# Performance work log

Hardware: AMD Instinct MI355X
Metric: run time of the kernel (lower is better)

The kernel has to match this reference:

```python
import jax, jax.numpy as jnp
import numpy as np

N_NODES = 100000
N_EDGES = 1600000
N_GRAPHS = 64
BN_EPS = 1e-5


def setup_inputs() -> dict:
    key = jax.random.key(0)
    ks = jax.random.split(key, 16)
    inp = {
        'x': jax.random.normal(ks[0], (N_NODES, 768), dtype=jnp.float32),
        'edge_index': jax.random.randint(ks[1], (2, N_EDGES), 0, N_NODES, dtype=jnp.int32),
        'batch': jnp.sort(jax.random.randint(ks[2], (N_NODES,), 0, N_GRAPHS, dtype=jnp.int32)),
        'W_in': jax.random.normal(ks[3], (768, 256), dtype=jnp.float32) * 0.02,
        'b_in': jax.random.normal(ks[4], (256,), dtype=jnp.float32) * 0.02,
        'W_g': jax.random.normal(ks[5], (3, 256, 256), dtype=jnp.float32) * 0.05,
        'b_g': jax.random.normal(ks[6], (3, 256), dtype=jnp.float32) * 0.02,
        'bn_gamma': jax.random.uniform(ks[7], (3, 256), dtype=jnp.float32) + 0.5,
        'bn_beta': jax.random.normal(ks[8], (3, 256), dtype=jnp.float32) * 0.02,
        'bn_mean': jax.random.normal(ks[9], (3, 256), dtype=jnp.float32) * 0.02,
        'bn_var': jax.random.uniform(ks[10], (3, 256), dtype=jnp.float32) + 0.5,
        'W1': jax.random.normal(ks[11], (256, 128), dtype=jnp.float32) * 0.06,
        'b1': jax.random.normal(ks[12], (128,), dtype=jnp.float32) * 0.02,
        'W2': jax.random.normal(ks[13], (128, 128), dtype=jnp.float32) * 0.08,
        'b2': jax.random.normal(ks[14], (128,), dtype=jnp.float32) * 0.02,
    }
    return inp


def reference(x, edge_index, batch, W_in, b_in, W_g, b_g, bn_gamma, bn_beta,
              bn_mean, bn_var, W1, b1, W2, b2):
    N = x.shape[0]
    # Add self loops (PyG GCNConv default)
    loop = jnp.arange(N, dtype=edge_index.dtype)
    src = jnp.concatenate([edge_index[0], loop])  # [E+N]
    dst = jnp.concatenate([edge_index[1], loop])
    # Symmetric GCN normalization: deg over dst after self loops
    deg = jax.ops.segment_sum(jnp.ones_like(src, dtype=x.dtype), dst, num_segments=N)
    dinv = jnp.where(deg > 0, jax.lax.rsqrt(deg), 0.0)
    norm = (dinv[src] * dinv[dst])[:, None]  # [E+N, 1]

    # input projection + relu
    h = jax.nn.relu(x @ W_in + b_in)  # [N, 256]

    for i in range(W_g.shape[0]):
        m = h @ W_g[i]                                   # [N, 256]
        agg = jax.ops.segment_sum(m[src] * norm, dst, num_segments=N) + b_g[i]
        # BatchNorm (eval mode, running stats)
        agg = (agg - bn_mean[i]) * (bn_gamma[i] * jax.lax.rsqrt(bn_var[i] + BN_EPS)) + bn_beta[i]
        h = jax.nn.relu(agg)  # dropout is identity in eval

    # global mean pool per graph
    sums = jax.ops.segment_sum(h, batch, num_segments=N_GRAPHS)       # [G, 256]
    cnts = jax.ops.segment_sum(jnp.ones((N,), x.dtype), batch, num_segments=N_GRAPHS)
    g = sums / jnp.maximum(cnts, 1.0)[:, None]

    # output MLP
    out = jax.nn.relu(g @ W1 + b1) @ W2 + b2  # [G, 128]
    return out
```

## Files before the change

### kernel.cpp

```cpp
#include <hip/hip_runtime.h>
#include <hip/hip_fp16.h>

#define HIDDEN 256

using bfrag = __attribute__((ext_vector_type(8))) short;
using facc4 = __attribute__((ext_vector_type(4))) float;

__device__ inline short bf16_rne(float x) {
  unsigned u = __builtin_bit_cast(unsigned, x);
  unsigned r = u + 0x7FFFu + ((u >> 16) & 1u);
  return (short)(r >> 16);
}
__device__ inline float bf16_to_f(short h) {
  unsigned u = ((unsigned)(unsigned short)h) << 16;
  return __builtin_bit_cast(float, u);
}
__device__ inline float h2f(unsigned short h) {
  return __half2float(__builtin_bit_cast(__half, h));
}

__global__ __launch_bounds__(256) void k_hist(const int* __restrict__ dst,
                                              int* __restrict__ deg, int E) {
  for (int e = blockIdx.x * blockDim.x + threadIdx.x; e < E;
       e += gridDim.x * blockDim.x)
    atomicAdd(&deg[dst[e]], 1);
}

__global__ __launch_bounds__(1024) void k_scan(const int* __restrict__ deg,
                                               int* __restrict__ row_ptr, int N) {
  __shared__ int wsum[16];
  __shared__ int carry;
  const int t = threadIdx.x, lane = t & 63, w = t >> 6;
  if (t == 0) { carry = 0; row_ptr[0] = 0; }
  __syncthreads();
  for (int base = 0; base < N; base += 1024) {
    const int idx = base + t;
    int x = (idx < N) ? deg[idx] : 0;
#pragma unroll
    for (int off = 1; off < 64; off <<= 1) {
      int y = __shfl_up(x, off);
      if (lane >= off) x += y;
    }
    if (lane == 63) wsum[w] = x;
    __syncthreads();
    if (w == 0 && lane < 16) {
      int s = wsum[lane];
#pragma unroll
      for (int off = 1; off < 16; off <<= 1) {
        int y = __shfl_up(s, off);
        if (lane >= off) s += y;
      }
      wsum[lane] = s;
    }
    __syncthreads();
    const int total = wsum[15];
    const int inc = carry + (w > 0 ? wsum[w - 1] : 0) + x;
    if (idx < N) row_ptr[idx + 1] = inc;
    __syncthreads();
    if (t == 0) carry += total;
  }
}

__global__ __launch_bounds__(256) void k_dinv(const int* __restrict__ deg,
                                              float* __restrict__ dinv, int N) {
  int v = blockIdx.x * blockDim.x + threadIdx.x;
  if (v < N) dinv[v] = 1.0f / sqrtf((float)deg[v] + 1.0f);
}

__global__ __launch_bounds__(256) void k_fill(const int* __restrict__ src,
                                              const int* __restrict__ dst,
                                              const int* __restrict__ row_ptr,
                                              int* __restrict__ fill,
                                              int* __restrict__ csr, int E) {
  for (int e = blockIdx.x * blockDim.x + threadIdx.x; e < E;
       e += gridDim.x * blockDim.x) {
    int d = dst[e];
    int pos = atomicAdd(&fill[d], 1);
    csr[row_ptr[d] + pos] = src[e];
  }
}

__global__ __launch_bounds__(256) void k_prep_w(const float* __restrict__ W_in,
                                                const float* __restrict__ W_g,
                                                short* __restrict__ Wt) {
  const int e = blockIdx.x * blockDim.x + threadIdx.x;
  if (e >= 196608 + 3 * 65536) return;
  float v;
  int k, n;
  size_t base;
  if (e < 196608) {
    k = e >> 8;
    n = e & 255;
    v = W_in[e];
    base = 0;
  } else {
    int r = e - 196608;
    int lyr = r >> 16;
    k = (r >> 8) & 255;
    n = r & 255;
    v = W_g[r];
    base = 393216 + (size_t)lyr * 131072;
  }
  size_t pos = base + (size_t)(k >> 5) * 16384 + (size_t)n * 32 + (k & 31);
  short hi = bf16_rne(v);
  short lo = bf16_rne(v - bf16_to_f(hi));
  Wt[pos] = hi;
  Wt[pos + 8192] = lo;
}

template <int EPI>
__global__ __launch_bounds__(256) void gemm_mfma(const float* __restrict__ A,
                                                 const short* __restrict__ Wt,
                                                 const float* __restrict__ aux,
                                                 float* __restrict__ C,
                                                 int M, int K) {
  __shared__ short As[2][64][72];
  const int t = threadIdx.x;
  const int w = t >> 6, l = t & 63;
  const int g = l >> 4, m16 = l & 15;
  const int row0 = blockIdx.x * 64;
  const int arow = t >> 2, ak = (t & 3) << 3;

  facc4 acc[4][4];
#pragma unroll
  for (int i = 0; i < 4; ++i)
#pragma unroll
    for (int j = 0; j < 4; ++j) acc[i][j] = (facc4)(0.0f);

  const int nsteps = K >> 5;
  const int ga = row0 + arow;
  const bool aval = ga < M;
  const float* aptr = A + (size_t)ga * K + ak;

  float4 f0 = make_float4(0.f, 0.f, 0.f, 0.f), f1 = f0;
  if (aval) {
    f0 = *(const float4*)(aptr);
    f1 = *(const float4*)(aptr + 4);
  }

  int cur = 0;
  for (int s = 0; s < nsteps; ++s) {
    float av[8] = {f0.x, f0.y, f0.z, f0.w, f1.x, f1.y, f1.z, f1.w};
    bfrag hif, lof;
#pragma unroll
    for (int i = 0; i < 8; ++i) {
      unsigned u = __builtin_bit_cast(unsigned, av[i]);
      hif[i] = (short)(u >> 16);
      float r = av[i] - __builtin_bit_cast(float, u & 0xFFFF0000u);
      lof[i] = (short)(__builtin_bit_cast(unsigned, r) >> 16);
    }
    *(bfrag*)&As[cur][arow][ak] = hif;
    *(bfrag*)&As[cur][arow][32 + ak] = lof;
    if (s + 1 < nsteps && aval) {
      f0 = *(const float4*)(aptr + (size_t)(s + 1) * 32);
      f1 = *(const float4*)(aptr + (size_t)(s + 1) * 32 + 4);
    }
    __syncthreads();
    const short* wb = Wt + ((size_t)s << 14) + (size_t)(w * 64 + m16) * 32 + g * 8;
    bfrag bh[4], bl[4];
#pragma unroll
    for (int nf = 0; nf < 4; ++nf) {
      bh[nf] = *(const bfrag*)(wb + nf * 512);
      bl[nf] = *(const bfrag*)(wb + nf * 512 + 8192);
    }
    bfrag ah[4], al[4];
#pragma unroll
    for (int mf = 0; mf < 4; ++mf) {
      ah[mf] = *(const bfrag*)&As[cur][mf * 16 + m16][g * 8];
      al[mf] = *(const bfrag*)&As[cur][mf * 16 + m16][32 + g * 8];
    }
#pragma unroll
    for (int nf = 0; nf < 4; ++nf)
#pragma unroll
      for (int mf = 0; mf < 4; ++mf)
        acc[mf][nf] = __builtin_amdgcn_mfma_f32_16x16x32_bf16(
            ah[mf], bh[nf], acc[mf][nf], 0, 0, 0);
#pragma unroll
    for (int nf = 0; nf < 4; ++nf)
#pragma unroll
      for (int mf = 0; mf < 4; ++mf)
        acc[mf][nf] = __builtin_amdgcn_mfma_f32_16x16x32_bf16(
            al[mf], bh[nf], acc[mf][nf], 0, 0, 0);
#pragma unroll
    for (int nf = 0; nf < 4; ++nf)
#pragma unroll
      for (int mf = 0; mf < 4; ++mf)
        acc[mf][nf] = __builtin_amdgcn_mfma_f32_16x16x32_bf16(
            ah[mf], bl[nf], acc[mf][nf], 0, 0, 0);
    cur ^= 1;
  }
  const int colbase = w * 64;
  if (EPI == 0) {
#pragma unroll
    for (int nf = 0; nf < 4; ++nf) {
      const float bias = aux[colbase + nf * 16 + m16];
#pragma unroll
      for (int mf = 0; mf < 4; ++mf)
#pragma unroll
        for (int r = 0; r < 4; ++r) {
          int row = row0 + mf * 16 + g * 4 + r;
          if (row < M)
            C[(size_t)row * HIDDEN + colbase + nf * 16 + m16] =
                fmaxf(acc[mf][nf][r] + bias, 0.f);
        }
    }
  } else {
    __half* Ch = (__half*)C;
#pragma unroll
    for (int mf = 0; mf < 4; ++mf)
#pragma unroll
      for (int r = 0; r < 4; ++r) {
        int row = row0 + mf * 16 + g * 4 + r;
        if (row >= M) continue;
        const float sc = aux[row];
#pragma unroll
        for (int nf = 0; nf < 4; ++nf)
          Ch[(size_t)row * HIDDEN + colbase + nf * 16 + m16] =
              __float2half(acc[mf][nf][r] * sc);
      }
  }
}

__global__ __launch_bounds__(256) void k_aggregate(
    const unsigned short* __restrict__ mp, const int* __restrict__ row_ptr,
    const int* __restrict__ csr, const float* __restrict__ dinv,
    const float* __restrict__ bg, const float* __restrict__ gamma,
    const float* __restrict__ beta, const float* __restrict__ mean,
    const float* __restrict__ var, float* __restrict__ hout, int N) {
  const int wave = threadIdx.x >> 6, l = threadIdx.x & 63;
  const int v = blockIdx.x * 4 + wave;
  if (v >= N) return;
  const int co = l << 2;
  ushort4 rs = *(const ushort4*)(mp + (size_t)v * HIDDEN + co);
  float4 acc;
  acc.x = h2f(rs.x); acc.y = h2f(rs.y); acc.z = h2f(rs.z); acc.w = h2f(rs.w);
  const int s = row_ptr[v], e = row_ptr[v + 1];
  int i = s;
  for (; i + 8 <= e; i += 8) {
    ushort4 r0 = *(const ushort4*)(mp + (size_t)csr[i + 0] * HIDDEN + co);
    ushort4 r1 = *(const ushort4*)(mp + (size_t)csr[i + 1] * HIDDEN + co);
    ushort4 r2 = *(const ushort4*)(mp + (size_t)csr[i + 2] * HIDDEN + co);
    ushort4 r3 = *(const ushort4*)(mp + (size_t)csr[i + 3] * HIDDEN + co);
    ushort4 r4 = *(const ushort4*)(mp + (size_t)csr[i + 4] * HIDDEN + co);
    ushort4 r5 = *(const ushort4*)(mp + (size_t)csr[i + 5] * HIDDEN + co);
    ushort4 r6 = *(const ushort4*)(mp + (size_t)csr[i + 6] * HIDDEN + co);
    ushort4 r7 = *(const ushort4*)(mp + (size_t)csr[i + 7] * HIDDEN + co);
    acc.x += h2f(r0.x) + h2f(r1.x) + h2f(r2.x) + h2f(r3.x) +
             h2f(r4.x) + h2f(r5.x) + h2f(r6.x) + h2f(r7.x);
    acc.y += h2f(r0.y) + h2f(r1.y) + h2f(r2.y) + h2f(r3.y) +
             h2f(r4.y) + h2f(r5.y) + h2f(r6.y) + h2f(r7.y);
    acc.z += h2f(r0.z) + h2f(r1.z) + h2f(r2.z) + h2f(r3.z) +
             h2f(r4.z) + h2f(r5.z) + h2f(r6.z) + h2f(r7.z);
    acc.w += h2f(r0.w) + h2f(r1.w) + h2f(r2.w) + h2f(r3.w) +
             h2f(r4.w) + h2f(r5.w) + h2f(r6.w) + h2f(r7.w);
  }
  for (; i < e; ++i) {
    ushort4 r0 = *(const ushort4*)(mp + (size_t)csr[i] * HIDDEN + co);
    acc.x += h2f(r0.x);
    acc.y += h2f(r0.y);
    acc.z += h2f(r0.z);
    acc.w += h2f(r0.w);
  }
  const float dv = dinv[v];
  float4 bg4 = *(const float4*)&bg[co];
  float4 g4 = *(const float4*)&gamma[co];
  float4 be4 = *(const float4*)&beta[co];
  float4 mn4 = *(const float4*)&mean[co];
  float4 vr4 = *(const float4*)&var[co];
  float4 o;
  o.x = fmaxf((acc.x * dv + bg4.x - mn4.x) * (g4.x / sqrtf(vr4.x + 1e-5f)) + be4.x, 0.f);
  o.y = fmaxf((acc.y * dv + bg4.y - mn4.y) * (g4.y / sqrtf(vr4.y + 1e-5f)) + be4.y, 0.f);
  o.z = fmaxf((acc.z * dv + bg4.z - mn4.z) * (g4.z / sqrtf(vr4.z + 1e-5f)) + be4.z, 0.f);
  o.w = fmaxf((acc.w * dv + bg4.w - mn4.w) * (g4.w / sqrtf(vr4.w + 1e-5f)) + be4.w, 0.f);
  ((float4*)hout)[(size_t)v * 64 + l] = o;
}

__global__ __launch_bounds__(64) void k_count(const int* __restrict__ batch,
                                              float* __restrict__ cnt, int N,
                                              int G) {
  const int g = threadIdx.x;
  if (g >= G) return;
  int lo = 0, hi = N;
  while (lo < hi) {
    int mid = (lo + hi) >> 1;
    if (batch[mid] < g) lo = mid + 1; else hi = mid;
  }
  int lo2 = lo, hi2 = N;
  while (lo2 < hi2) {
    int mid = (lo2 + hi2) >> 1;
    if (batch[mid] < g + 1) lo2 = mid + 1; else hi2 = mid;
  }
  cnt[g] = (float)(lo2 - lo);
}

__global__ __launch_bounds__(256) void k_pool(const float* __restrict__ h,
                                              const int* __restrict__ batch,
                                              float* __restrict__ sums, int N) {
  const int t = threadIdx.x;
  const int start = blockIdx.x * 256;
  if (start >= N) return;
  const int end = min(start + 256, N);
  float acc = 0.f;
  int cur = batch[start];
  for (int n = start; n < end; ++n) {
    int g = batch[n];
    if (g != cur) {
      atomicAdd(&sums[cur * HIDDEN + t], acc);
      acc = 0.f;
      cur = g;
    }
    acc += h[(size_t)n * HIDDEN + t];
  }
  atomicAdd(&sums[cur * HIDDEN + t], acc);
}

__global__ __launch_bounds__(128) void k_head(const float* __restrict__ sums,
                                              const float* __restrict__ cnt,
                                              const float* __restrict__ W1,
                                              const float* __restrict__ b1,
                                              const float* __restrict__ W2,
                                              const float* __restrict__ b2,
                                              float* __restrict__ out) {
  __shared__ float gr[256];
  __shared__ float t1[128];
  const int b = blockIdx.x, t = threadIdx.x;
  const float inv = 1.0f / fmaxf(cnt[b], 1.0f);
  gr[t] = sums[b * HIDDEN + t] * inv;
  gr[t + 128] = sums[b * HIDDEN + t + 128] * inv;
  __syncthreads();
  float a = b1[t];
  for (int k = 0; k < 256; ++k) a += gr[k] * W1[k * 128 + t];
  t1[t] = fmaxf(a, 0.f);
  __syncthreads();
  float o = b2[t];
  for (int k = 0; k < 128; ++k) o += t1[k] * W2[k * 128 + t];
  out[b * 128 + t] = o;
}

extern "C" void kernel_launch(void* const* d_in, const int* in_sizes, int n_in,
                              void* d_out, int out_size, void* d_ws,
                              size_t ws_size, hipStream_t stream) {
  (void)n_in;
  (void)ws_size;
  const float* x = (const float*)d_in[0];
  const int* ei = (const int*)d_in[1];
  const int* batch = (const int*)d_in[2];
  const float* W_in = (const float*)d_in[3];
  const float* b_in = (const float*)d_in[4];
  const float* W_g = (const float*)d_in[5];
  const float* b_g = (const float*)d_in[6];
  const float* bn_gamma = (const float*)d_in[7];
  const float* bn_beta = (const float*)d_in[8];
  const float* bn_mean = (const float*)d_in[9];
  const float* bn_var = (const float*)d_in[10];
  const float* W1 = (const float*)d_in[11];
  const float* b1 = (const float*)d_in[12];
  const float* W2 = (const float*)d_in[13];
  const float* b2 = (const float*)d_in[14];

  const int KIN = 768;
  const int N = in_sizes[0] / KIN;
  const int E = in_sizes[1] / 2;
  const int G = out_size / 128;

  const int* src = ei;
  const int* dst = ei + E;

  char* ws = (char*)d_ws;
  size_t off = 0;
  auto take = [&](size_t bytes) -> void* {
    void* p = ws + off;
    off += (bytes + 255) & ~(size_t)255;
    return p;
  };
  float* h0 = (float*)take((size_t)N * HIDDEN * 4);
  unsigned short* h1 = (unsigned short*)take((size_t)N * HIDDEN * 2);
  float* dinv = (float*)take((size_t)N * 4);
  int* deg = (int*)take((size_t)N * 4);
  int* fill = (int*)take((size_t)N * 4);
  int* row_ptr = (int*)take((size_t)(N + 1) * 4);
  int* csr = (int*)take((size_t)E * 4);
  float* sums = (float*)take((size_t)G * HIDDEN * 4);
  float* cnt = (float*)take((size_t)G * 4);
  short* Wt = (short*)take((size_t)(393216 + 3 * 131072) * 2);

  hipMemsetAsync(deg, 0, (size_t)N * 4, stream);
  hipMemsetAsync(fill, 0, (size_t)N * 4, stream);
  hipMemsetAsync(sums, 0, (size_t)G * HIDDEN * 4, stream);

  k_prep_w<<<(196608 + 3 * 65536 + 255) / 256, 256, 0, stream>>>(W_in, W_g, Wt);
  k_hist<<<2048, 256, 0, stream>>>(dst, deg, E);
  k_scan<<<1, 1024, 0, stream>>>(deg, row_ptr, N);
  k_dinv<<<(N + 255) / 256, 256, 0, stream>>>(deg, dinv, N);
  k_fill<<<2048, 256, 0, stream>>>(src, dst, row_ptr, fill, csr, E);

  const int gx = (N + 63) / 64;
  gemm_mfma<0><<<gx, 256, 0, stream>>>(x, Wt, b_in, h0, N, KIN);
  for (int i = 0; i < 3; ++i) {
    gemm_mfma<1><<<gx, 256, 0, stream>>>(h0, Wt + 393216 + (size_t)i * 131072,
                                         dinv, (float*)h1, N, HIDDEN);
    k_aggregate<<<(N + 3) / 4, 256, 0, stream>>>(
        h1, row_ptr, csr, dinv, b_g + i * HIDDEN, bn_gamma + i * HIDDEN,
        bn_beta + i * HIDDEN, bn_mean + i * HIDDEN, bn_var + i * HIDDEN, h0, N);
  }
  k_count<<<1, 64, 0, stream>>>(batch, cnt, N, G);
  k_pool<<<(N + 255) / 256, 256, 0, stream>>>(h0, batch, sums, N);
  k_head<<<G, 128, 0, stream>>>(sums, cnt, W1, b1, W2, b2, (float*)d_out);
}
```

Before: 1.105 ms.

## Parallelize CSR scan across blocks and enlarge GEMM tile to 128 rows

```diff
diff --git a/kernel.cpp b/kernel.cpp
--- a/kernel.cpp
+++ b/kernel.cpp
@@ -17,6 +17,16 @@
 }
 __device__ inline float h2f(unsigned short h) {
   return __half2float(__builtin_bit_cast(__half, h));
+}
+__device__ inline void cvt8(const float4& a, const float4& b, bfrag& hi, bfrag& lo) {
+  float av[8] = {a.x, a.y, a.z, a.w, b.x, b.y, b.z, b.w};
+#pragma unroll
+  for (int i = 0; i < 8; ++i) {
+    unsigned u = __builtin_bit_cast(unsigned, av[i]);
+    hi[i] = (short)(u >> 16);
+    float r = av[i] - __builtin_bit_cast(float, u & 0xFFFF0000u);
+    lo[i] = (short)(__builtin_bit_cast(unsigned, r) >> 16);
+  }
 }
 
 __global__ __launch_bounds__(256) void k_hist(const int* __restrict__ dst,
@@ -26,45 +36,71 @@
     atomicAdd(&deg[dst[e]], 1);
 }
 
-__global__ __launch_bounds__(1024) void k_scan(const int* __restrict__ deg,
-                                               int* __restrict__ row_ptr, int N) {
-  __shared__ int wsum[16];
-  __shared__ int carry;
+__global__ __launch_bounds__(256) void k_scan_a(const int* __restrict__ deg,
+                                                int* __restrict__ bsum, int N) {
   const int t = threadIdx.x, lane = t & 63, w = t >> 6;
-  if (t == 0) { carry = 0; row_ptr[0] = 0; }
-  __syncthreads();
-  for (int base = 0; base < N; base += 1024) {
-    const int idx = base + t;
-    int x = (idx < N) ? deg[idx] : 0;
-#pragma unroll
-    for (int off = 1; off < 64; off <<= 1) {
-      int y = __shfl_up(x, off);
-      if (lane >= off) x += y;
-    }
-    if (lane == 63) wsum[w] = x;
-    __syncthreads();
-    if (w == 0 && lane < 16) {
-      int s = wsum[lane];
-#pragma unroll
-      for (int off = 1; off < 16; off <<= 1) {
-        int y = __shfl_up(s, off);
-        if (lane >= off) s += y;
-      }
-      wsum[lane] = s;
-    }
-    __syncthreads();
-    const int total = wsum[15];
-    const int inc = carry + (w > 0 ? wsum[w - 1] : 0) + x;
-    if (idx < N) row_ptr[idx + 1] = inc;
-    __syncthreads();
-    if (t == 0) carry += total;
-  }
-}
-
-__global__ __launch_bounds__(256) void k_dinv(const int* __restrict__ deg,
-                                              float* __restrict__ dinv, int N) {
-  int v = blockIdx.x * blockDim.x + threadIdx.x;
-  if (v < N) dinv[v] = 1.0f / sqrtf((float)deg[v] + 1.0f);
+  const int idx = blockIdx.x * 256 + t;
+  int x = (idx < N) ? deg[idx] : 0;
+#pragma unroll
+  for (int off = 32; off >= 1; off >>= 1) x += __shfl_xor(x, off);
+  __shared__ int ws[4];
+  if (lane == 0) ws[w] = x;
+  __syncthreads();
+  if (t == 0) bsum[blockIdx.x] = ws[0] + ws[1] + ws[2] + ws[3];
+}
+
+__global__ __launch_bounds__(512) void k_scan_b(const int* __restrict__ bsum,
+                                                int* __restrict__ boff, int nb) {
+  const int t = threadIdx.x, lane = t & 63, w = t >> 6;
+  int orig = (t < nb) ? bsum[t] : 0;
+  int x = orig;
+#pragma unroll
+  for (int off = 1; off < 64; off <<= 1) {
+    int y = __shfl_up(x, off);
+    if (lane >= off) x += y;
+  }
+  __shared__ int wsum[8];
+  if (lane == 63) wsum[w] = x;
+  __syncthreads();
+  if (w == 0 && lane < 8) {
+    int s = wsum[lane];
+#pragma unroll
+    for (int off = 1; off < 8; off <<= 1) {
+      int y = __shfl_up(s, off);
+      if (lane >= off) s += y;
+    }
+    wsum[lane] = s;
+  }
+  __syncthreads();
+  int inc = x + (w > 0 ? wsum[w - 1] : 0);
+  if (t < nb) boff[t] = inc - orig;
+}
+
+__global__ __launch_bounds__(256) void k_scan_c(const int* __restrict__ deg,
+                                                const int* __restrict__ boff,
+                                                int* __restrict__ row_ptr,
+                                                float* __restrict__ dinv, int N) {
+  const int t = threadIdx.x, lane = t & 63, w = t >> 6;
+  const int idx = blockIdx.x * 256 + t;
+  int d = (idx < N) ? deg[idx] : 0;
+  int x = d;
+#pragma unroll
+  for (int off = 1; off < 64; off <<= 1) {
+    int y = __shfl_up(x, off);
+    if (lane >= off) x += y;
+  }
+  __shared__ int ws[4];
+  if (lane == 63) ws[w] = x;
+  __syncthreads();
+  int add = boff[blockIdx.x];
+#pragma unroll
+  for (int j = 0; j < 4; ++j)
+    if (j < w) add += ws[j];
+  if (idx < N) {
+    row_ptr[idx + 1] = x + add;
+    dinv[idx] = 1.0f / sqrtf((float)d + 1.0f);
+  }
+  if (idx == 0) row_ptr[0] = 0;
 }
 
 __global__ __launch_bounds__(256) void k_fill(const int* __restrict__ src,
@@ -109,17 +145,19 @@
 }
 
 template <int EPI>
-__global__ __launch_bounds__(256) void gemm_mfma(const float* __restrict__ A,
-                                                 const short* __restrict__ Wt,
-                                                 const float* __restrict__ aux,
-                                                 float* __restrict__ C,
-                                                 int M, int K) {
-  __shared__ short As[2][64][72];
+__global__ __launch_bounds__(512, 4) void gemm_mfma(const float* __restrict__ A,
+                                                    const short* __restrict__ Wt,
+                                                    const float* __restrict__ aux,
+                                                    float* __restrict__ C,
+                                                    int M, int K) {
+  __shared__ short As[2][128][72];
   const int t = threadIdx.x;
   const int w = t >> 6, l = t & 63;
   const int g = l >> 4, m16 = l & 15;
-  const int row0 = blockIdx.x * 64;
-  const int arow = t >> 2, ak = (t & 3) << 3;
+  const int wr = w >> 2, wc = w & 3;
+  const int row0 = blockIdx.x * 128;
+  const int arow = t >> 2;
+  const int ks = (t & 3) << 3;
 
   facc4 acc[4][4];
 #pragma unroll
@@ -130,66 +168,71 @@
   const int nsteps = K >> 5;
   const int ga = row0 + arow;
   const bool aval = ga < M;
-  const float* aptr = A + (size_t)ga * K + ak;
+  const float* aptr = A + (size_t)ga * K + ks;
 
   float4 f0 = make_float4(0.f, 0.f, 0.f, 0.f), f1 = f0;
   if (aval) {
-    f0 = *(const float4*)(aptr);
+    f0 = *(const float4*)(aptr + 0);
     f1 = *(const float4*)(aptr + 4);
+  }
+  {
+    bfrag hi, lo;
+    cvt8(f0, f1, hi, lo);
+    *(bfrag*)&As[0][arow][ks] = hi;
+    *(bfrag*)&As[0][arow][32 + ks] = lo;
   }
 
   int cur = 0;
   for (int s = 0; s < nsteps; ++s) {
-    float av[8] = {f0.x, f0.y, f0.z, f0.w, f1.x, f1.y, f1.z, f1.w};
-    bfrag hif, lof;
-#pragma unroll
-    for (int i = 0; i < 8; ++i) {
-      unsigned u = __builtin_bit_cast(unsigned, av[i]);
-      hif[i] = (short)(u >> 16);
-      float r = av[i] - __builtin_bit_cast(float, u & 0xFFFF0000u);
-      lof[i] = (short)(__builtin_bit_cast(unsigned, r) >> 16);
-    }
-    *(bfrag*)&As[cur][arow][ak] = hif;
-    *(bfrag*)&As[cur][arow][32 + ak] = lof;
-    if (s + 1 < nsteps && aval) {
-      f0 = *(const float4*)(aptr + (size_t)(s + 1) * 32);
-      f1 = *(const float4*)(aptr + (size_t)(s + 1) * 32 + 4);
-    }
     __syncthreads();
-    const short* wb = Wt + ((size_t)s << 14) + (size_t)(w * 64 + m16) * 32 + g * 8;
+    const bool havenext = (s + 1 < nsteps);
+    if (havenext && aval) {
+      const float* ap = aptr + (size_t)(s + 1) * 32;
+      f0 = *(const float4*)(ap + 0);
+      f1 = *(const float4*)(ap + 4);
+    }
+    const short* wb = Wt + ((size_t)s << 14) + (size_t)(wc * 64 + m16) * 32 + g * 8;
     bfrag bh[4], bl[4];
 #pragma unroll
     for (int nf = 0; nf < 4; ++nf) {
       bh[nf] = *(const bfrag*)(wb + nf * 512);
       bl[nf] = *(const bfrag*)(wb + nf * 512 + 8192);
     }
-    bfrag ah[4], al[4];
-#pragma unroll
-    for (int mf = 0; mf < 4; ++mf) {
-      ah[mf] = *(const bfrag*)&As[cur][mf * 16 + m16][g * 8];
-      al[mf] = *(const bfrag*)&As[cur][mf * 16 + m16][32 + g * 8];
-    }
+    bfrag af[4];
+#pragma unroll
+    for (int mf = 0; mf < 4; ++mf)
+      af[mf] = *(const bfrag*)&As[cur][wr * 64 + mf * 16 + m16][g * 8];
 #pragma unroll
     for (int nf = 0; nf < 4; ++nf)
 #pragma unroll
       for (int mf = 0; mf < 4; ++mf)
         acc[mf][nf] = __builtin_amdgcn_mfma_f32_16x16x32_bf16(
-            ah[mf], bh[nf], acc[mf][nf], 0, 0, 0);
+            af[mf], bh[nf], acc[mf][nf], 0, 0, 0);
 #pragma unroll
     for (int nf = 0; nf < 4; ++nf)
 #pragma unroll
       for (int mf = 0; mf < 4; ++mf)
         acc[mf][nf] = __builtin_amdgcn_mfma_f32_16x16x32_bf16(
-            al[mf], bh[nf], acc[mf][nf], 0, 0, 0);
+            af[mf], bl[nf], acc[mf][nf], 0, 0, 0);
+#pragma unroll
+    for (int mf = 0; mf < 4; ++mf)
+      af[mf] = *(const bfrag*)&As[cur][wr * 64 + mf * 16 + m16][32 + g * 8];
 #pragma unroll
     for (int nf = 0; nf < 4; ++nf)
 #pragma unroll
       for (int mf = 0; mf < 4; ++mf)
         acc[mf][nf] = __builtin_amdgcn_mfma_f32_16x16x32_bf16(
-            ah[mf], bl[nf], acc[mf][nf], 0, 0, 0);
+            af[mf], bh[nf], acc[mf][nf], 0, 0, 0);
+    if (havenext) {
+      bfrag hi, lo;
+      cvt8(f0, f1, hi, lo);
+      *(bfrag*)&As[cur ^ 1][arow][ks] = hi;
+      *(bfrag*)&As[cur ^ 1][arow][32 + ks] = lo;
+    }
     cur ^= 1;
   }
-  const int colbase = w * 64;
+  const int colbase = wc * 64;
+  const int rowbase = row0 + wr * 64;
   if (EPI == 0) {
 #pragma unroll
     for (int nf = 0; nf < 4; ++nf) {
@@ -198,7 +241,7 @@
       for (int mf = 0; mf < 4; ++mf)
 #pragma unroll
         for (int r = 0; r < 4; ++r) {
-          int row = row0 + mf * 16 + g * 4 + r;
+          int row = rowbase + mf * 16 + g * 4 + r;
           if (row < M)
             C[(size_t)row * HIDDEN + colbase + nf * 16 + m16] =
                 fmaxf(acc[mf][nf][r] + bias, 0.f);
@@ -210,7 +253,7 @@
     for (int mf = 0; mf < 4; ++mf)
 #pragma unroll
       for (int r = 0; r < 4; ++r) {
-        int row = row0 + mf * 16 + g * 4 + r;
+        int row = rowbase + mf * 16 + g * 4 + r;
         if (row >= M) continue;
         const float sc = aux[row];
 #pragma unroll
@@ -383,6 +426,9 @@
   float* sums = (float*)take((size_t)G * HIDDEN * 4);
   float* cnt = (float*)take((size_t)G * 4);
   short* Wt = (short*)take((size_t)(393216 + 3 * 131072) * 2);
+  const int nb = (N + 255) / 256;
+  int* bsum = (int*)take((size_t)nb * 4);
+  int* boff = (int*)take((size_t)nb * 4);
 
   hipMemsetAsync(deg, 0, (size_t)N * 4, stream);
   hipMemsetAsync(fill, 0, (size_t)N * 4, stream);
@@ -390,14 +436,15 @@
 
   k_prep_w<<<(196608 + 3 * 65536 + 255) / 256, 256, 0, stream>>>(W_in, W_g, Wt);
   k_hist<<<2048, 256, 0, stream>>>(dst, deg, E);
-  k_scan<<<1, 1024, 0, stream>>>(deg, row_ptr, N);
-  k_dinv<<<(N + 255) / 256, 256, 0, stream>>>(deg, dinv, N);
+  k_scan_a<<<nb, 256, 0, stream>>>(deg, bsum, N);
+  k_scan_b<<<1, 512, 0, stream>>>(bsum, boff, nb);
+  k_scan_c<<<nb, 256, 0, stream>>>(deg, boff, row_ptr, dinv, N);
   k_fill<<<2048, 256, 0, stream>>>(src, dst, row_ptr, fill, csr, E);
 
-  const int gx = (N + 63) / 64;
-  gemm_mfma<0><<<gx, 256, 0, stream>>>(x, Wt, b_in, h0, N, KIN);
+  const int gx = (N + 127) / 128;
+  gemm_mfma<0><<<gx, 512, 0, stream>>>(x, Wt, b_in, h0, N, KIN);
   for (int i = 0; i < 3; ++i) {
-    gemm_mfma<1><<<gx, 256, 0, stream>>>(h0, Wt + 393216 + (size_t)i * 131072,
+    gemm_mfma<1><<<gx, 512, 0, stream>>>(h0, Wt + 393216 + (size_t)i * 131072,
                                          dinv, (float*)h1, N, HIDDEN);
     k_aggregate<<<(N + 3) / 4, 256, 0, stream>>>(
         h1, row_ptr, csr, dinv, b_g + i * HIDDEN, bn_gamma + i * HIDDEN,
```

After: 1.161 ms. +5.1%, slower.
